# Optimization experiments

Measured on AMD Instinct MI355X. Metric: run time of the kernel, lower is better.

## Reference

```python
import jax, jax.numpy as jnp
import numpy as np

B, T, H, DIN, DOUT = 512, 256, 512, 514, 2
DT_OVER_TAU = 1.0 / 10.0

def retanh(a):
    return jnp.maximum(jnp.tanh(a), 0.0)

def setup_inputs() -> dict:
    key = jax.random.key(0)
    ks = jax.random.split(key, 5)
    x = jax.random.normal(ks[0], (B, T, DIN), dtype=jnp.float32)
    noise = jax.random.normal(ks[1], (B, T, H), dtype=jnp.float32) * 0.1
    W_x_ah = jax.random.normal(ks[2], (H, DIN), dtype=jnp.float32) / np.sqrt(DIN).astype(np.float32)
    b_ah = jnp.zeros((H,), dtype=jnp.float32)
    W_h_ah = jax.random.normal(ks[3], (H, H), dtype=jnp.float32) / np.sqrt(H).astype(np.float32)
    W_h_y = jnp.zeros((DOUT, H), dtype=jnp.float32)
    ah0 = jnp.zeros((H,), dtype=jnp.float32)
    return {"x": x, "noise": noise, "W_x_ah": W_x_ah, "b_ah": b_ah,
            "W_h_ah": W_h_ah, "W_h_y": W_h_y, "ah0": ah0}

def reference(x, noise, W_x_ah, b_ah, W_h_ah, W_h_y, ah0):
    batch = x.shape[0]
    # precompute input drive for all timesteps: [B,T,H]
    x2ah = jnp.einsum('btd,hd->bth', x, W_x_ah) + b_ah
    ah_init = jnp.broadcast_to(ah0, (batch, H))
    h_init = retanh(ah_init)

    def step(carry, inp):
        ah, h = carry
        xt, nt = inp  # [B,H], [B,H]
        ah = ah + DT_OVER_TAU * (-ah + h @ W_h_ah.T + xt)
        h = retanh(ah) + nt
        return (ah, h), h

    xs = (jnp.swapaxes(x2ah, 0, 1), jnp.swapaxes(noise, 0, 1))  # [T,B,H]
    _, hs = jax.lax.scan(step, (ah_init, h_init), xs)
    hstore = jnp.swapaxes(hs, 0, 1)  # [B,T,H]
    output = jnp.einsum('bth,oh->bto', hstore, W_h_y)
    return output, hstore
```

## Files before the change

kernel.cpp:

```cpp
#include <hip/hip_runtime.h>
#include <math.h>

#define BB   512
#define TT   256
#define HH   512
#define DIN  514
#define DOUTN 2
#define DT   0.1f
#define TH   (TT * HH)

#define NSL   4
#define NGRP  32

typedef short s16x8 __attribute__((ext_vector_type(8)));
typedef float f32x4 __attribute__((ext_vector_type(4)));

__device__ __forceinline__ float retanh_f(float a) {
    float am = fminf(a, 15.0f);
    float E  = __expf(2.0f * am);
    float tp = __fdividef(E - 1.0f, E + 1.0f);
    return a > 0.0f ? tp : 0.0f;
}

__device__ __forceinline__ unsigned short f2bf(float f) {
    unsigned u = __float_as_uint(f);
    unsigned r = (u + 0x7FFFu + ((u >> 16) & 1u)) >> 16;
    return (unsigned short)r;
}

__global__ __launch_bounds__(256) void pack_wh(const float* __restrict__ Wh,
                                               unsigned short* __restrict__ Wp) {
    const int idx = blockIdx.x * 256 + threadIdx.x;
    const int l  = idx & 63;
    const int jt = (idx >> 6) & 31;
    const int kc = idx >> 11;
    const int j  = jt * 16 + (l & 15);
    const int k0 = kc * 32 + (l >> 4) * 8;
    s16x8 pv;
    #pragma unroll
    for (int e = 0; e < 8; ++e) pv[e] = (short)f2bf(Wh[j * HH + k0 + e]);
    *(s16x8*)&Wp[(size_t)idx * 8] = pv;
}

__global__ __launch_bounds__(256) void pack_wx(const float* __restrict__ Wx,
                                               unsigned short* __restrict__ WfH,
                                               unsigned short* __restrict__ WfL) {
    const int idx = blockIdx.x * 256 + threadIdx.x;
    const int l  = idx & 63;
    const int jt = (idx >> 6) & 31;
    const int kc = idx >> 11;
    const int j  = jt * 16 + (l & 15);
    const int k0 = kc * 32 + (l >> 4) * 8;
    s16x8 ph, pl;
    #pragma unroll
    for (int e = 0; e < 8; ++e) {
        const float v = Wx[(size_t)j * DIN + k0 + e];
        const unsigned short hi = f2bf(v);
        const float hv = __uint_as_float((unsigned)hi << 16);
        ph[e] = (short)hi;
        pl[e] = (short)f2bf(v - hv);
    }
    *(s16x8*)&WfH[(size_t)idx * 8] = ph;
    *(s16x8*)&WfL[(size_t)idx * 8] = pl;
}

__global__ __launch_bounds__(512) void x2ah_mfma(const float* __restrict__ X,
                                                 const unsigned short* __restrict__ WfH,
                                                 const unsigned short* __restrict__ WfL,
                                                 const float* __restrict__ Wx,
                                                 const float* __restrict__ bias,
                                                 const float* __restrict__ noise,
                                                 unsigned int* __restrict__ outp) {
    __shared__ __align__(16) char arena[5120 + 5120 + 512 + 65536];
    unsigned short* xh = (unsigned short*)arena;
    unsigned short* xl = xh + 64 * 40;
    float*          xt = (float*)(xl + 64 * 40);
    s16x8*         wsh = (s16x8*)(xt + 128);
    s16x8*         wsl = wsh + 2048;
    unsigned short* ls = (unsigned short*)wsh;

    const int tid = threadIdx.x;
    const int l   = tid & 63;
    const int w   = tid >> 6;
    const int lm  = l & 15;
    const int lg  = l >> 4;
    const int lg4 = lg * 4;
    const int r0  = blockIdx.x * 64;

    const int rt  = w & 3;
    const int jt0 = (w >> 2) * 16;

    if (tid < 128) {
        const int row = tid >> 1, c2 = tid & 1;
        xt[row * 2 + c2] = X[(size_t)(r0 + row) * DIN + 512 + c2];
    }

    f32x4 acc[16];
    #pragma unroll
    for (int jt = 0; jt < 16; ++jt) acc[jt] = (f32x4){0.f, 0.f, 0.f, 0.f};

    const s16x8* WfHv = (const s16x8*)WfH;
    const s16x8* WfLv = (const s16x8*)WfL;

    for (int kc = 0; kc < 16; ++kc) {
        {
            const int row = tid >> 3, q = tid & 7;
            const float* xp = X + (size_t)(r0 + row) * DIN + kc * 32 + q * 4;
            const float2 v0 = *(const float2*)xp;
            const float2 v1 = *(const float2*)(xp + 2);
            float vv[4] = {v0.x, v0.y, v1.x, v1.y};
            ushort4 hh, llv;
            unsigned short* hp = (unsigned short*)&hh;
            unsigned short* lp = (unsigned short*)&llv;
            #pragma unroll
            for (int e = 0; e < 4; ++e) {
                const unsigned short hi = f2bf(vv[e]);
                hp[e] = hi;
                lp[e] = f2bf(vv[e] - __uint_as_float((unsigned)hi << 16));
            }
            *(ushort4*)&xh[row * 40 + q * 4] = hh;
            *(ushort4*)&xl[row * 40 + q * 4] = llv;
        }
        {
            const size_t base = (size_t)kc * 2048 + tid * 4;
            wsh[tid * 4 + 0] = WfHv[base + 0];
            wsh[tid * 4 + 1] = WfHv[base + 1];
            wsh[tid * 4 + 2] = WfHv[base + 2];
            wsh[tid * 4 + 3] = WfHv[base + 3];
            wsl[tid * 4 + 0] = WfLv[base + 0];
            wsl[tid * 4 + 1] = WfLv[base + 1];
            wsl[tid * 4 + 2] = WfLv[base + 2];
            wsl[tid * 4 + 3] = WfLv[base + 3];
        }
        __syncthreads();

        const s16x8 Ah = *(const s16x8*)&xh[(rt * 16 + lm) * 40 + lg * 8];
        const s16x8 Al = *(const s16x8*)&xl[(rt * 16 + lm) * 40 + lg * 8];
        #pragma unroll
        for (int jt = 0; jt < 16; ++jt) {
            const s16x8 Bh = wsh[(jt0 + jt) * 64 + l];
            const s16x8 Bl = wsl[(jt0 + jt) * 64 + l];
            acc[jt] = __builtin_amdgcn_mfma_f32_16x16x32_bf16(Ah, Bh, acc[jt], 0, 0, 0);
            acc[jt] = __builtin_amdgcn_mfma_f32_16x16x32_bf16(Al, Bh, acc[jt], 0, 0, 0);
            acc[jt] = __builtin_amdgcn_mfma_f32_16x16x32_bf16(Ah, Bl, acc[jt], 0, 0, 0);
        }
        __syncthreads();
    }

    for (int c = 0; c < 4; ++c) {
        if (rt == c) {
            #pragma unroll
            for (int jt = 0; jt < 16; ++jt) {
                const int j = (jt0 + jt) * 16 + lm;
                const float2 wt = *(const float2*)&Wx[(size_t)j * DIN + 512];
                const float bj = bias[j];
                #pragma unroll
                for (int r = 0; r < 4; ++r) {
                    const int rl = lg4 + r;
                    const float v = acc[jt][r] + bj
                                  + xt[(c * 16 + rl) * 2 + 0] * wt.x
                                  + xt[(c * 16 + rl) * 2 + 1] * wt.y;
                    ls[rl * 512 + j] = f2bf(v);
                }
            }
        }
        __syncthreads();
        {
            const int i   = tid * 16;
            const int row = i >> 9, col = i & 511;
            const size_t gi = (size_t)(r0 + c * 16 + row) * HH + col;
            const float4 n0 = *(const float4*)&noise[gi + 0];
            const float4 n1 = *(const float4*)&noise[gi + 4];
            const float4 n2 = *(const float4*)&noise[gi + 8];
            const float4 n3 = *(const float4*)&noise[gi + 12];
            const unsigned short* lp = &ls[row * 512 + col];
            const uint4 la = *(const uint4*)lp;
            const uint4 lb = *(const uint4*)(lp + 8);
            uint4 o0, o1, o2, o3;
            o0.x = ((la.x & 0xffffu) << 16) | f2bf(n0.x);
            o0.y = (la.x & 0xffff0000u)     | f2bf(n0.y);
            o0.z = ((la.y & 0xffffu) << 16) | f2bf(n0.z);
            o0.w = (la.y & 0xffff0000u)     | f2bf(n0.w);
            o1.x = ((la.z & 0xffffu) << 16) | f2bf(n1.x);
            o1.y = (la.z & 0xffff0000u)     | f2bf(n1.y);
            o1.z = ((la.w & 0xffffu) << 16) | f2bf(n1.z);
            o1.w = (la.w & 0xffff0000u)     | f2bf(n1.w);
            o2.x = ((lb.x & 0xffffu) << 16) | f2bf(n2.x);
            o2.y = (lb.x & 0xffff0000u)     | f2bf(n2.y);
            o2.z = ((lb.y & 0xffffu) << 16) | f2bf(n2.z);
            o2.w = (lb.y & 0xffff0000u)     | f2bf(n2.w);
            o3.x = ((lb.z & 0xffffu) << 16) | f2bf(n3.x);
            o3.y = (lb.z & 0xffff0000u)     | f2bf(n3.y);
            o3.z = ((lb.w & 0xffffu) << 16) | f2bf(n3.z);
            o3.w = (lb.w & 0xffff0000u)     | f2bf(n3.w);
            *(uint4*)&outp[gi + 0]  = o0;
            *(uint4*)&outp[gi + 4]  = o1;
            *(uint4*)&outp[gi + 8]  = o2;
            *(uint4*)&outp[gi + 12] = o3;
        }
        __syncthreads();
    }
}

#define WKLOAD(KC) s16x8 wk##KC = WpV[((KC) * 32 + s * 8 + w) * 64 + l]
#define WKPIN(A, B, C, D) asm volatile("" : "+v"(A), "+v"(B), "+v"(C), "+v"(D))

#define KC_EVEN(KC) do { \
    const s16x8 A = *(const s16x8*)&hrow[(KC) * 32]; \
    accA = __builtin_amdgcn_mfma_f32_16x16x32_bf16(A, wk##KC, accA, 0, 0, 0); \
} while (0)
#define KC_ODD(KC) do { \
    const s16x8 A = *(const s16x8*)&hrow[(KC) * 32]; \
    accB = __builtin_amdgcn_mfma_f32_16x16x32_bf16(A, wk##KC, accB, 0, 0, 0); \
} while (0)

__global__ __launch_bounds__(512) void scan12_kernel(const unsigned short* __restrict__ Wp,
                                                     const float* __restrict__ ah0,
                                                     unsigned int* __restrict__ hio,
                                                     unsigned short* inbox,
                                                     unsigned int* flags) {
    __shared__ __align__(16) unsigned short hs[16][520];

    const int tid = threadIdx.x;
    const int l   = tid & 63;
    const int w   = tid >> 6;
    const int lm  = l & 15;
    const int lg  = l >> 4;
    const int lg4 = lg * 4;
    const int gid = blockIdx.x;
    const int g   = gid >> 2;
    const int s   = gid & 3;
    const int b0  = g * 16;

    const s16x8* WpV = (const s16x8*)Wp;

    WKLOAD(0);  WKLOAD(1);  WKLOAD(2);  WKLOAD(3);
    WKLOAD(4);  WKLOAD(5);  WKLOAD(6);  WKLOAD(7);
    WKLOAD(8);  WKLOAD(9);  WKLOAD(10); WKLOAD(11);
    WKLOAD(12); WKLOAD(13); WKLOAD(14); WKLOAD(15);
    WKPIN(wk0, wk1, wk2, wk3);     WKPIN(wk4, wk5, wk6, wk7);
    WKPIN(wk8, wk9, wk10, wk11);   WKPIN(wk12, wk13, wk14, wk15);

    const int jn = (s * 8 + w) * 16 + lm;

    f32x4 ahv;
    {
        const float a0 = ah0[jn];
        ahv = (f32x4){a0, a0, a0, a0};
    }

    for (int idx = tid; idx < 16 * 512; idx += 512) {
        int b = idx >> 9, k = idx & 511;
        hs[b][k] = f2bf(retanh_f(ah0[k]));
    }
    __syncthreads();

    const unsigned short* hrow = &hs[lm][lg * 8];

    const int pb = tid >> 5;
    const int pq = tid & 31;
    unsigned long long* ibx = (unsigned long long*)inbox;
    const int pubIdx = (((b0 + pb) << 9) + s * 128 + pq * 4) >> 2;
    const int gatIdx = (((b0 + pb) << 9) + pq * 16) >> 2;

    int gb = (b0 + lg4) * TH + jn;

    for (int t = 0; t < TT; ++t) {
        const int par = (t & 1) << 16;

        const unsigned int pk0 = hio[gb + 0 * TH];
        const unsigned int pk1 = hio[gb + 1 * TH];
        const unsigned int pk2 = hio[gb + 2 * TH];
        const unsigned int pk3 = hio[gb + 3 * TH];

        f32x4 accA = (f32x4){0.f, 0.f, 0.f, 0.f};
        f32x4 accB = (f32x4){0.f, 0.f, 0.f, 0.f};
        KC_EVEN(0);  KC_ODD(1);  KC_EVEN(2);  KC_ODD(3);
        KC_EVEN(4);  KC_ODD(5);  KC_EVEN(6);  KC_ODD(7);
        KC_EVEN(8);  KC_ODD(9);  KC_EVEN(10); KC_ODD(11);
        KC_EVEN(12); KC_ODD(13); KC_EVEN(14); KC_ODD(15);
        const f32x4 acc = accA + accB;

        __syncthreads();

        {
            float a, h;
            unsigned int p;
            p = pk0; a = ahv[0];
            a += DT * (acc[0] + __uint_as_float(p & 0xffff0000u) - a);
            ahv[0] = a; h = retanh_f(a) + __uint_as_float(p << 16);
            hio[gb + 0 * TH] = __float_as_uint(h); hs[lg4 + 0][jn] = f2bf(h);
            p = pk1; a = ahv[1];
            a += DT * (acc[1] + __uint_as_float(p & 0xffff0000u) - a);
            ahv[1] = a; h = retanh_f(a) + __uint_as_float(p << 16);
            hio[gb + 1 * TH] = __float_as_uint(h); hs[lg4 + 1][jn] = f2bf(h);
            p = pk2; a = ahv[2];
            a += DT * (acc[2] + __uint_as_float(p & 0xffff0000u) - a);
            ahv[2] = a; h = retanh_f(a) + __uint_as_float(p << 16);
            hio[gb + 2 * TH] = __float_as_uint(h); hs[lg4 + 2][jn] = f2bf(h);
            p = pk3; a = ahv[3];
            a += DT * (acc[3] + __uint_as_float(p & 0xffff0000u) - a);
            ahv[3] = a; h = retanh_f(a) + __uint_as_float(p << 16);
            hio[gb + 3 * TH] = __float_as_uint(h); hs[lg4 + 3][jn] = f2bf(h);
        }

        __syncthreads();

        {
            const unsigned long long pub =
                *(const unsigned long long*)&hs[pb][s * 128 + pq * 4];
            __hip_atomic_store(&ibx[par + pubIdx], pub, __ATOMIC_RELAXED,
                               __HIP_MEMORY_SCOPE_AGENT);
        }
        asm volatile("s_waitcnt vmcnt(0)" ::: "memory");
        __syncthreads();

        unsigned int* fl = flags + (t * NGRP + g) * NSL;
        if (tid == 0)
            __hip_atomic_store(&fl[s], 1u, __ATOMIC_RELAXED, __HIP_MEMORY_SCOPE_AGENT);
        if (tid < NSL) {
            while (__hip_atomic_load(&fl[tid], __ATOMIC_RELAXED,
                                     __HIP_MEMORY_SCOPE_AGENT) == 0u)
                __builtin_amdgcn_s_sleep(1);
        }
        __syncthreads();

        {
            const unsigned long long g0 = __hip_atomic_load(&ibx[par + gatIdx + 0],
                __ATOMIC_RELAXED, __HIP_MEMORY_SCOPE_AGENT);
            const unsigned long long g1 = __hip_atomic_load(&ibx[par + gatIdx + 1],
                __ATOMIC_RELAXED, __HIP_MEMORY_SCOPE_AGENT);
            const unsigned long long g2 = __hip_atomic_load(&ibx[par + gatIdx + 2],
                __ATOMIC_RELAXED, __HIP_MEMORY_SCOPE_AGENT);
            const unsigned long long g3 = __hip_atomic_load(&ibx[par + gatIdx + 3],
                __ATOMIC_RELAXED, __HIP_MEMORY_SCOPE_AGENT);
            *(unsigned long long*)&hs[pb][pq * 16 + 0]  = g0;
            *(unsigned long long*)&hs[pb][pq * 16 + 4]  = g1;
            *(unsigned long long*)&hs[pb][pq * 16 + 8]  = g2;
            *(unsigned long long*)&hs[pb][pq * 16 + 12] = g3;
        }
        __syncthreads();

        gb += HH;
    }
}

__global__ __launch_bounds__(256) void out_kernel(const float* __restrict__ hstore,
                                                  const float* __restrict__ Wy,
                                                  float* __restrict__ out0) {
    const int wave = threadIdx.x >> 6;
    const int lane = threadIdx.x & 63;
    const int r = blockIdx.x * 4 + wave;

    const float4* hv4 = (const float4*)&hstore[r * HH];
    float a0 = 0.0f, a1 = 0.0f;
    #pragma unroll
    for (int u = 0; u < 2; ++u) {
        const int e = u * 64 + lane;
        const float4 h  = hv4[e];
        const float4 w0 = *(const float4*)&Wy[e * 4];
        const float4 w1 = *(const float4*)&Wy[HH + e * 4];
        a0 += h.x * w0.x + h.y * w0.y + h.z * w0.z + h.w * w0.w;
        a1 += h.x * w1.x + h.y * w1.y + h.z * w1.z + h.w * w1.w;
    }
    #pragma unroll
    for (int off = 32; off > 0; off >>= 1) {
        a0 += __shfl_xor(a0, off);
        a1 += __shfl_xor(a1, off);
    }
    if (lane == 0) {
        out0[r * 2]     = a0;
        out0[r * 2 + 1] = a1;
    }
}

extern "C" void kernel_launch(void* const* d_in, const int* in_sizes, int n_in,
                              void* d_out, int out_size, void* d_ws, size_t ws_size,
                              hipStream_t stream) {
    const float* x     = (const float*)d_in[0];
    const float* noise = (const float*)d_in[1];
    const float* Wx    = (const float*)d_in[2];
    const float* bah   = (const float*)d_in[3];
    const float* Wh    = (const float*)d_in[4];
    const float* Wy    = (const float*)d_in[5];
    const float* ah0   = (const float*)d_in[6];

    float* out0   = (float*)d_out;
    float* hstore = (float*)d_out + BB * TT * DOUTN;

    const size_t FRAG_U16 = (size_t)16 * 32 * 64 * 8;
    unsigned short* Wp    = (unsigned short*)d_ws;
    unsigned short* WxH   = Wp + FRAG_U16;
    unsigned short* WxL   = WxH + FRAG_U16;
    unsigned short* inbox = WxL + FRAG_U16;
    unsigned int*   flags = (unsigned int*)(inbox + 2 * BB * HH);

    pack_wh<<<16 * 32 * 64 / 256, 256, 0, stream>>>(Wh, Wp);
    pack_wx<<<16 * 32 * 64 / 256, 256, 0, stream>>>(Wx, WxH, WxL);
    x2ah_mfma<<<BB * TT / 64, 512, 0, stream>>>(x, WxH, WxL, Wx, bah, noise,
                                                (unsigned int*)hstore);

    hipMemsetAsync(flags, 0, (size_t)TT * NGRP * NSL * sizeof(unsigned int), stream);
    {
        const unsigned short* wpp = Wp;
        unsigned int* hiop = (unsigned int*)hstore;
        unsigned short* ibp = inbox;
        unsigned int* flp = flags;
        void* args[] = { (void*)&wpp, (void*)&ah0, (void*)&hiop,
                         (void*)&ibp, (void*)&flp };
        hipLaunchCooperativeKernel((void*)scan12_kernel, dim3(NGRP * NSL),
                                   dim3(512), args, 0, stream);
    }

    out_kernel<<<BB * TT / 4, 256, 0, stream>>>(hstore, Wy, out0);
}
```

Before: 1.378 ms.

## Double-buffer x2ah weight staging via direct LDS loads and prefetch scan inputs

```diff
diff --git a/kernel.cpp b/kernel.cpp
--- a/kernel.cpp
+++ b/kernel.cpp
@@ -26,6 +26,12 @@
     unsigned u = __float_as_uint(f);
     unsigned r = (u + 0x7FFFu + ((u >> 16) & 1u)) >> 16;
     return (unsigned short)r;
+}
+
+__device__ __forceinline__ void gload_lds16(const void* g, void* l) {
+    __builtin_amdgcn_global_load_lds(
+        (const __attribute__((address_space(1))) unsigned int*)g,
+        (__attribute__((address_space(3))) unsigned int*)l, 16, 0, 0);
 }
 
 __global__ __launch_bounds__(256) void pack_wh(const float* __restrict__ Wh,
@@ -64,6 +70,31 @@
     *(s16x8*)&WfL[(size_t)idx * 8] = pl;
 }
 
+__device__ __forceinline__ void cvt_hilo(float4 a, float4 b, s16x8& hi, s16x8& lo) {
+    float v[8] = {a.x, a.y, a.z, a.w, b.x, b.y, b.z, b.w};
+    #pragma unroll
+    for (int e = 0; e < 8; ++e) {
+        const unsigned short h = f2bf(v[e]);
+        hi[e] = (short)h;
+        lo[e] = (short)f2bf(v[e] - __uint_as_float((unsigned)h << 16));
+    }
+}
+
+#define STAGE_W(KC, DST) do { \
+    const s16x8* gh = WfHv + (size_t)(KC) * 2048 + w * 256 + l; \
+    const s16x8* gl = WfLv + (size_t)(KC) * 2048 + w * 256 + l; \
+    s16x8* dh = (DST) + w * 256; \
+    s16x8* dl = (DST) + 2048 + w * 256; \
+    gload_lds16(gh + 0 * 64, dh + 0 * 64); \
+    gload_lds16(gh + 1 * 64, dh + 1 * 64); \
+    gload_lds16(gh + 2 * 64, dh + 2 * 64); \
+    gload_lds16(gh + 3 * 64, dh + 3 * 64); \
+    gload_lds16(gl + 0 * 64, dl + 0 * 64); \
+    gload_lds16(gl + 1 * 64, dl + 1 * 64); \
+    gload_lds16(gl + 2 * 64, dl + 2 * 64); \
+    gload_lds16(gl + 3 * 64, dl + 3 * 64); \
+} while (0)
+
 __global__ __launch_bounds__(512) void x2ah_mfma(const float* __restrict__ X,
                                                  const unsigned short* __restrict__ WfH,
                                                  const unsigned short* __restrict__ WfL,
@@ -71,13 +102,7 @@
                                                  const float* __restrict__ bias,
                                                  const float* __restrict__ noise,
                                                  unsigned int* __restrict__ outp) {
-    __shared__ __align__(16) char arena[5120 + 5120 + 512 + 65536];
-    unsigned short* xh = (unsigned short*)arena;
-    unsigned short* xl = xh + 64 * 40;
-    float*          xt = (float*)(xl + 64 * 40);
-    s16x8*         wsh = (s16x8*)(xt + 128);
-    s16x8*         wsl = wsh + 2048;
-    unsigned short* ls = (unsigned short*)wsh;
+    __shared__ __align__(16) char arena[2][65536];
 
     const int tid = threadIdx.x;
     const int l   = tid & 63;
@@ -85,70 +110,72 @@
     const int lm  = l & 15;
     const int lg  = l >> 4;
     const int lg4 = lg * 4;
-    const int r0  = blockIdx.x * 64;
+    const int lg8 = lg * 8;
+    const int r0  = blockIdx.x * 128;
 
     const int rt  = w & 3;
     const int jt0 = (w >> 2) * 16;
 
-    if (tid < 128) {
-        const int row = tid >> 1, c2 = tid & 1;
-        xt[row * 2 + c2] = X[(size_t)(r0 + row) * DIN + 512 + c2];
-    }
-
-    f32x4 acc[16];
-    #pragma unroll
-    for (int jt = 0; jt < 16; ++jt) acc[jt] = (f32x4){0.f, 0.f, 0.f, 0.f};
-
     const s16x8* WfHv = (const s16x8*)WfH;
     const s16x8* WfLv = (const s16x8*)WfL;
 
+    const float* xr0 = X + (size_t)(r0 + rt * 32 + lm) * DIN;
+    const float* xr1 = xr0 + 16 * DIN;
+
+    float4 xa0 = *(const float4*)(xr0 + lg8);
+    float4 xb0 = *(const float4*)(xr0 + lg8 + 4);
+    float4 xa1 = *(const float4*)(xr1 + lg8);
+    float4 xb1 = *(const float4*)(xr1 + lg8 + 4);
+    STAGE_W(0, (s16x8*)arena[0]);
+    __syncthreads();
+
+    f32x4 acc0[16], acc1[16];
+    #pragma unroll
+    for (int jt = 0; jt < 16; ++jt) {
+        acc0[jt] = (f32x4){0.f, 0.f, 0.f, 0.f};
+        acc1[jt] = (f32x4){0.f, 0.f, 0.f, 0.f};
+    }
+
     for (int kc = 0; kc < 16; ++kc) {
-        {
-            const int row = tid >> 3, q = tid & 7;
-            const float* xp = X + (size_t)(r0 + row) * DIN + kc * 32 + q * 4;
-            const float2 v0 = *(const float2*)xp;
-            const float2 v1 = *(const float2*)(xp + 2);
-            float vv[4] = {v0.x, v0.y, v1.x, v1.y};
-            ushort4 hh, llv;
-            unsigned short* hp = (unsigned short*)&hh;
-            unsigned short* lp = (unsigned short*)&llv;
-            #pragma unroll
-            for (int e = 0; e < 4; ++e) {
-                const unsigned short hi = f2bf(vv[e]);
-                hp[e] = hi;
-                lp[e] = f2bf(vv[e] - __uint_as_float((unsigned)hi << 16));
-            }
-            *(ushort4*)&xh[row * 40 + q * 4] = hh;
-            *(ushort4*)&xl[row * 40 + q * 4] = llv;
-        }
-        {
-            const size_t base = (size_t)kc * 2048 + tid * 4;
-            wsh[tid * 4 + 0] = WfHv[base + 0];
-            wsh[tid * 4 + 1] = WfHv[base + 1];
-            wsh[tid * 4 + 2] = WfHv[base + 2];
-            wsh[tid * 4 + 3] = WfHv[base + 3];
-            wsl[tid * 4 + 0] = WfLv[base + 0];
-            wsl[tid * 4 + 1] = WfLv[base + 1];
-            wsl[tid * 4 + 2] = WfLv[base + 2];
-            wsl[tid * 4 + 3] = WfLv[base + 3];
-        }
-        __syncthreads();
-
-        const s16x8 Ah = *(const s16x8*)&xh[(rt * 16 + lm) * 40 + lg * 8];
-        const s16x8 Al = *(const s16x8*)&xl[(rt * 16 + lm) * 40 + lg * 8];
+        s16x8* cur = (s16x8*)arena[kc & 1];
+        s16x8* nxt = (s16x8*)arena[(kc & 1) ^ 1];
+        if (kc < 15) STAGE_W(kc + 1, nxt);
+
+        s16x8 Ah0, Al0, Ah1, Al1;
+        cvt_hilo(xa0, xb0, Ah0, Al0);
+        cvt_hilo(xa1, xb1, Ah1, Al1);
+        if (kc < 15) {
+            const int off = (kc + 1) * 32 + lg8;
+            xa0 = *(const float4*)(xr0 + off);
+            xb0 = *(const float4*)(xr0 + off + 4);
+            xa1 = *(const float4*)(xr1 + off);
+            xb1 = *(const float4*)(xr1 + off + 4);
+        }
+
         #pragma unroll
         for (int jt = 0; jt < 16; ++jt) {
-            const s16x8 Bh = wsh[(jt0 + jt) * 64 + l];
-            const s16x8 Bl = wsl[(jt0 + jt) * 64 + l];
-            acc[jt] = __builtin_amdgcn_mfma_f32_16x16x32_bf16(Ah, Bh, acc[jt], 0, 0, 0);
-            acc[jt] = __builtin_amdgcn_mfma_f32_16x16x32_bf16(Al, Bh, acc[jt], 0, 0, 0);
-            acc[jt] = __builtin_amdgcn_mfma_f32_16x16x32_bf16(Ah, Bl, acc[jt], 0, 0, 0);
-        }
-        __syncthreads();
-    }
-
-    for (int c = 0; c < 4; ++c) {
-        if (rt == c) {
+            const s16x8 Bh = cur[(jt0 + jt) * 64 + l];
+            const s16x8 Bl = cur[2048 + (jt0 + jt) * 64 + l];
+            acc0[jt] = __builtin_amdgcn_mfma_f32_16x16x32_bf16(Ah0, Bh, acc0[jt], 0, 0, 0);
+            acc0[jt] = __builtin_amdgcn_mfma_f32_16x16x32_bf16(Al0, Bh, acc0[jt], 0, 0, 0);
+            acc0[jt] = __builtin_amdgcn_mfma_f32_16x16x32_bf16(Ah0, Bl, acc0[jt], 0, 0, 0);
+            acc1[jt] = __builtin_amdgcn_mfma_f32_16x16x32_bf16(Ah1, Bh, acc1[jt], 0, 0, 0);
+            acc1[jt] = __builtin_amdgcn_mfma_f32_16x16x32_bf16(Al1, Bh, acc1[jt], 0, 0, 0);
+            acc1[jt] = __builtin_amdgcn_mfma_f32_16x16x32_bf16(Ah1, Bl, acc1[jt], 0, 0, 0);
+        }
+        __syncthreads();
+    }
+
+    unsigned short* ls = (unsigned short*)arena;
+    for (int c = 0; c < 8; ++c) {
+        if (rt == (c >> 1)) {
+            float xt0[4], xt1[4];
+            #pragma unroll
+            for (int r = 0; r < 4; ++r) {
+                const float* xrow = X + (size_t)(r0 + c * 16 + lg4 + r) * DIN + 512;
+                xt0[r] = xrow[0];
+                xt1[r] = xrow[1];
+            }
             #pragma unroll
             for (int jt = 0; jt < 16; ++jt) {
                 const int j = (jt0 + jt) * 16 + lm;
@@ -156,11 +183,9 @@
                 const float bj = bias[j];
                 #pragma unroll
                 for (int r = 0; r < 4; ++r) {
-                    const int rl = lg4 + r;
-                    const float v = acc[jt][r] + bj
-                                  + xt[(c * 16 + rl) * 2 + 0] * wt.x
-                                  + xt[(c * 16 + rl) * 2 + 1] * wt.y;
-                    ls[rl * 512 + j] = f2bf(v);
+                    const float av = (c & 1) ? acc1[jt][r] : acc0[jt][r];
+                    const float v = av + bj + xt0[r] * wt.x + xt1[r] * wt.y;
+                    ls[(lg4 + r) * 512 + j] = f2bf(v);
                 }
             }
         }
@@ -261,17 +286,17 @@
     const int pq = tid & 31;
     unsigned long long* ibx = (unsigned long long*)inbox;
     const int pubIdx = (((b0 + pb) << 9) + s * 128 + pq * 4) >> 2;
-    const int gatIdx = (((b0 + pb) << 9) + pq * 16) >> 2;
+    const int gatIdx = ((b0 + pb) << 7) + pq;
 
     int gb = (b0 + lg4) * TH + jn;
+
+    unsigned int pk0 = hio[gb + 0 * TH];
+    unsigned int pk1 = hio[gb + 1 * TH];
+    unsigned int pk2 = hio[gb + 2 * TH];
+    unsigned int pk3 = hio[gb + 3 * TH];
 
     for (int t = 0; t < TT; ++t) {
         const int par = (t & 1) << 16;
-
-        const unsigned int pk0 = hio[gb + 0 * TH];
-        const unsigned int pk1 = hio[gb + 1 * TH];
-        const unsigned int pk2 = hio[gb + 2 * TH];
-        const unsigned int pk3 = hio[gb + 3 * TH];
 
         f32x4 accA = (f32x4){0.f, 0.f, 0.f, 0.f};
         f32x4 accB = (f32x4){0.f, 0.f, 0.f, 0.f};
@@ -318,6 +343,14 @@
         unsigned int* fl = flags + (t * NGRP + g) * NSL;
         if (tid == 0)
             __hip_atomic_store(&fl[s], 1u, __ATOMIC_RELAXED, __HIP_MEMORY_SCOPE_AGENT);
+
+        if (t + 1 < TT) {
+            pk0 = hio[gb + HH + 0 * TH];
+            pk1 = hio[gb + HH + 1 * TH];
+            pk2 = hio[gb + HH + 2 * TH];
+            pk3 = hio[gb + HH + 3 * TH];
+        }
+
         if (tid < NSL) {
             while (__hip_atomic_load(&fl[tid], __ATOMIC_RELAXED,
                                      __HIP_MEMORY_SCOPE_AGENT) == 0u)
@@ -326,18 +359,18 @@
         __syncthreads();
 
         {
-            const unsigned long long g0 = __hip_atomic_load(&ibx[par + gatIdx + 0],
+            const unsigned long long g0 = __hip_atomic_load(&ibx[par + gatIdx + 0 * 32],
                 __ATOMIC_RELAXED, __HIP_MEMORY_SCOPE_AGENT);
-            const unsigned long long g1 = __hip_atomic_load(&ibx[par + gatIdx + 1],
+            const unsigned long long g1 = __hip_atomic_load(&ibx[par + gatIdx + 1 * 32],
                 __ATOMIC_RELAXED, __HIP_MEMORY_SCOPE_AGENT);
-            const unsigned long long g2 = __hip_atomic_load(&ibx[par + gatIdx + 2],
+            const unsigned long long g2 = __hip_atomic_load(&ibx[par + gatIdx + 2 * 32],
                 __ATOMIC_RELAXED, __HIP_MEMORY_SCOPE_AGENT);
-            const unsigned long long g3 = __hip_atomic_load(&ibx[par + gatIdx + 3],
+            const unsigned long long g3 = __hip_atomic_load(&ibx[par + gatIdx + 3 * 32],
                 __ATOMIC_RELAXED, __HIP_MEMORY_SCOPE_AGENT);
-            *(unsigned long long*)&hs[pb][pq * 16 + 0]  = g0;
-            *(unsigned long long*)&hs[pb][pq * 16 + 4]  = g1;
-            *(unsigned long long*)&hs[pb][pq * 16 + 8]  = g2;
-            *(unsigned long long*)&hs[pb][pq * 16 + 12] = g3;
+            *(unsigned long long*)&hs[pb][pq * 4 + 0 * 128] = g0;
+            *(unsigned long long*)&hs[pb][pq * 4 + 1 * 128] = g1;
+            *(unsigned long long*)&hs[pb][pq * 4 + 2 * 128] = g2;
+            *(unsigned long long*)&hs[pb][pq * 4 + 3 * 128] = g3;
         }
         __syncthreads();
 
@@ -397,8 +430,8 @@
 
     pack_wh<<<16 * 32 * 64 / 256, 256, 0, stream>>>(Wh, Wp);
     pack_wx<<<16 * 32 * 64 / 256, 256, 0, stream>>>(Wx, WxH, WxL);
-    x2ah_mfma<<<BB * TT / 64, 512, 0, stream>>>(x, WxH, WxL, Wx, bah, noise,
-                                                (unsigned int*)hstore);
+    x2ah_mfma<<<BB * TT / 128, 512, 0, stream>>>(x, WxH, WxL, Wx, bah, noise,
+                                                 (unsigned int*)hstore);
 
     hipMemsetAsync(flags, 0, (size_t)TT * NGRP * NSL * sizeof(unsigned int), stream);
     {
```

New measurement: 1.119 ms. -18.8%, faster.
